# Performance work log

Hardware: AMD Instinct MI355X
Metric: run time of the kernel (lower is better)

The kernel has to match this reference:

```python
import jax, jax.numpy as jnp
import numpy as np

B_, C, N, M, DX = 4, 8, 1024, 1024, 1
POINTS_PER_UNIT = 64


def setup_inputs() -> dict:
    key = jax.random.key(0)
    k1, k2, k3 = jax.random.split(key, 3)
    xz = jax.random.uniform(k1, (M, DX), dtype=jnp.float32)          # grid locations
    z = jax.random.normal(k2, (B_, C, M, M), dtype=jnp.float32)      # grid encoding
    x = jax.random.normal(k3, (B_, N, DX), dtype=jnp.float32)        # target locations
    log_scale = jnp.log(jnp.float32(2.0 / POINTS_PER_UNIT))          # learned scalar
    return {"xz": xz, "z": z, "x": x, "log_scale": log_scale}


def reference(xz, z, x, log_scale):
    # pairwise squared distances: (b, n, m)
    dists2 = jnp.sum((x[:, :, None, :] - xz[None, None, :, :]) ** 2, axis=-1)
    # RBF weights
    weights = jnp.exp(-0.5 * dists2 / jnp.exp(2.0 * log_scale))      # (b, n, m)
    # weighted interpolation of grid encoding: (b, c, n, m)
    z1 = jnp.einsum("bnm,bcmk->bcnk", weights, z)
    # outer product z1 @ z1^T: (b, c, n, n)
    z2 = jnp.einsum("bcnk,bcok->bcno", z1, z1)
    return (xz, z2)
```

## Files before the change

kernel.cpp:

```cpp
#include <hip/hip_runtime.h>
#include <hip/hip_bf16.h>


typedef __attribute__((ext_vector_type(8))) unsigned short u16x8;
typedef __attribute__((ext_vector_type(8))) __bf16 bf16x8;
typedef __attribute__((ext_vector_type(4))) float f32x4;

typedef __attribute__((address_space(1))) void gvoid;
typedef __attribute__((address_space(3))) void svoid;
#define GLDS(g, s) __builtin_amdgcn_global_load_lds((gvoid*)(g), (svoid*)(s), 16, 0, 0)
#define BAR() asm volatile("s_barrier" ::: "memory")

__device__ __forceinline__ unsigned short f2bf(float f) {
  unsigned int u = __builtin_bit_cast(unsigned int, f);
  u += 0x7fffu + ((u >> 16) & 1u);
  return (unsigned short)(u >> 16);
}

__device__ __forceinline__ bf16x8 as_bf16x8(u16x8 v) {
  return __builtin_bit_cast(bf16x8, v);
}

__global__ void weights_kernel(const float* __restrict__ xz, const float* __restrict__ x,
                               const float* __restrict__ ls, unsigned short* __restrict__ W) {
  int bn = blockIdx.x;
  float xv = x[bn];
  float coef = -0.5f * __expf(-2.0f * ls[0]);
  unsigned short* Wrow = W + (size_t)bn * 1024;
  #pragma unroll
  for (int i = 0; i < 4; ++i) {
    int m = threadIdx.x + i * 256;
    float d = xv - xz[m];
    Wrow[m] = f2bf(__expf(coef * d * d));
  }
}

__global__ void transpose_kernel(const float* __restrict__ Z, unsigned short* __restrict__ Zt) {
  __shared__ float tile[64][65];
  int bc = blockIdx.z;
  const float* Zp = Z + ((size_t)bc << 20);
  unsigned short* Ztp = Zt + ((size_t)bc << 20);
  int m0 = blockIdx.x * 64, k0 = blockIdx.y * 64;
  int tx = threadIdx.x & 63, tg = threadIdx.x >> 6;
  #pragma unroll
  for (int i = 0; i < 16; ++i) {
    int ml = tg + i * 4;
    tile[ml][tx] = Zp[(size_t)(m0 + ml) * 1024 + k0 + tx];
  }
  __syncthreads();
  int tx2 = (threadIdx.x & 31) * 2, kg = threadIdx.x >> 5;
  #pragma unroll
  for (int i = 0; i < 8; ++i) {
    int kl = kg + i * 8;
    ushort2 v;
    v.x = f2bf(tile[tx2][kl]);
    v.y = f2bf(tile[tx2 + 1][kl]);
    *(ushort2*)&Ztp[(size_t)(k0 + kl) * 1024 + m0 + tx2] = v;
  }
}

template<bool A_PER_B>
__global__ __launch_bounds__(512, 2)
void gemm_nt8(const unsigned short* __restrict__ A, const unsigned short* __restrict__ B,
              unsigned short* __restrict__ Cbf) {
  extern __shared__ __align__(16) char smem[];

  const int bid = blockIdx.x;
  const int w = ((bid & 7) << 6) + (bid >> 3);
  const int bc = w >> 4;
  const int t  = w & 15;
  const int bi = t & 3, bj = t >> 2;

  const unsigned short* Ap = A + ((size_t)(A_PER_B ? (bc >> 3) : bc) << 20);
  const unsigned short* Bp = B + ((size_t)bc << 20);
  const int tid = threadIdx.x;
  const int wv = tid >> 6, lane = tid & 63;
  const int wr = wv >> 2, wc = wv & 3;
  const int la = lane & 15, ha = lane >> 4;

  f32x4 acc[8][4] = {};

  const int slog = (lane & 7) ^ (lane >> 3);
  const int rloc = 2 * (lane >> 3) + (slog & 1);
  const int cloc = (slog >> 1) * 8;
  const unsigned short* gA0 = Ap + (size_t)(bi*256 +       wv*16 + rloc) * 1024 + cloc;
  const unsigned short* gA1 = Ap + (size_t)(bi*256 + 128 + wv*16 + rloc) * 1024 + cloc;
  const unsigned short* gB0 = Bp + (size_t)(bj*256 +       wv*16 + rloc) * 1024 + cloc;
  const unsigned short* gB1 = Bp + (size_t)(bj*256 + 128 + wv*16 + rloc) * 1024 + cloc;
  const int ldsw = wv * 1024;

  auto stageA = [&](int d, int kh, int kt) {
    const int ko = kt * 64 + kh * 32;
    char* dst = smem + d * 32768 + kh * 16384 + ldsw;
    GLDS(gA0 + ko, dst); GLDS(gA1 + ko, dst + 8192);
  };
  auto stageB = [&](int d, int kh, int kt) {
    const int ko = kt * 64 + kh * 32;
    char* dst = smem + 65536 + d * 32768 + kh * 16384 + ldsw;
    GLDS(gB0 + ko, dst); GLDS(gB1 + ko, dst + 8192);
  };

  const int sphys = ((ha << 1) | (la & 1)) ^ (la >> 1);
  const int abase = wr * 8192 + (la >> 1) * 128 + sphys * 16;
  const int bbase = 65536 + wc * 4096 + (la >> 1) * 128 + sphys * 16;

  u16x8 aX[4], aY[4], b0[4], b1[4];
  auto lda4 = [&](u16x8* dst, int d, int kh, int ms) {
    const char* p = smem + d * 32768 + kh * 16384 + ms * 4096 + abase;
    dst[0] = *(const u16x8*)(p);
    dst[1] = *(const u16x8*)(p + 1024);
    dst[2] = *(const u16x8*)(p + 2048);
    dst[3] = *(const u16x8*)(p + 3072);
  };
  auto ldb4 = [&](u16x8* dst, int d, int kh) {
    const char* p = smem + d * 32768 + kh * 16384 + bbase;
    dst[0] = *(const u16x8*)(p);
    dst[1] = *(const u16x8*)(p + 1024);
    dst[2] = *(const u16x8*)(p + 2048);
    dst[3] = *(const u16x8*)(p + 3072);
  };
  auto mfma16 = [&](const u16x8* Af, const u16x8* Bf, int ms) {
    __builtin_amdgcn_s_setprio(1);
    #pragma unroll
    for (int i = 0; i < 4; ++i)
      #pragma unroll
      for (int n = 0; n < 4; ++n)
        acc[ms * 4 + i][n] = __builtin_amdgcn_mfma_f32_16x16x32_bf16(
            as_bf16x8(Af[i]), as_bf16x8(Bf[n]), acc[ms * 4 + i][n], 0, 0, 0);
    __builtin_amdgcn_s_setprio(0);
  };

  stageA(0, 0, 0); stageB(0, 0, 0);
  stageA(0, 1, 0); stageB(0, 1, 0);
  stageA(1, 0, 1); stageB(1, 0, 1);
  asm volatile("s_waitcnt vmcnt(8)" ::: "memory");
  BAR();
  ldb4(b0, 0, 0); lda4(aX, 0, 0, 0);

  for (int tt = 0; tt < 14; ++tt) {
    const int d = tt & 1;
    stageA(d ^ 1, 1, tt + 1);
    lda4(aY, d, 0, 1);
    mfma16(aX, b0, 0);
    stageB(d ^ 1, 1, tt + 1);
    asm volatile("s_waitcnt vmcnt(8)" ::: "memory");
    BAR();
    ldb4(b1, d, 1); lda4(aX, d, 1, 0);
    mfma16(aY, b0, 1);
    stageA(d, 0, tt + 2);
    lda4(aY, d, 1, 1);
    mfma16(aX, b1, 0);
    stageB(d, 0, tt + 2);
    asm volatile("s_waitcnt vmcnt(8)" ::: "memory");
    BAR();
    ldb4(b0, d ^ 1, 0); lda4(aX, d ^ 1, 0, 0);
    mfma16(aY, b1, 1);
  }
  stageA(1, 1, 15);
  lda4(aY, 0, 0, 1);
  mfma16(aX, b0, 0);
  stageB(1, 1, 15);
  asm volatile("s_waitcnt vmcnt(8)" ::: "memory");
  BAR();
  ldb4(b1, 0, 1); lda4(aX, 0, 1, 0);
  mfma16(aY, b0, 1);
  lda4(aY, 0, 1, 1);
  mfma16(aX, b1, 0);
  asm volatile("s_waitcnt vmcnt(4)" ::: "memory");
  BAR();
  ldb4(b0, 1, 0); lda4(aX, 1, 0, 0);
  mfma16(aY, b1, 1);
  lda4(aY, 1, 0, 1);
  mfma16(aX, b0, 0);
  asm volatile("s_waitcnt vmcnt(0)" ::: "memory");
  BAR();
  ldb4(b1, 1, 1); lda4(aX, 1, 1, 0);
  mfma16(aY, b0, 1);
  lda4(aY, 1, 1, 1);
  mfma16(aX, b1, 0);
  mfma16(aY, b1, 1);
  BAR();

  const size_t cb20 = (size_t)bc << 20;
  unsigned short* sE = (unsigned short*)(smem) + wv * 1152;
  const int r2 = lane >> 2, ch = lane & 3;
  #pragma unroll
  for (int mb = 0; mb < 8; ++mb) {
    #pragma unroll
    for (int nb = 0; nb < 4; ++nb)
      #pragma unroll
      for (int j = 0; j < 4; ++j)
        sE[(ha * 4 + j) * 72 + nb * 16 + la] = f2bf(acc[mb][nb][j]);
    u16x8 v0 = *(const u16x8*)&sE[r2 * 72 + ch * 16];
    u16x8 v1 = *(const u16x8*)&sE[r2 * 72 + ch * 16 + 8];
    unsigned short* gp = Cbf + cb20 +
        (size_t)(bi * 256 + wr * 128 + mb * 16 + r2) * 1024 + bj * 256 + wc * 64 + ch * 16;
    *(u16x8*)gp = v0;
    *(u16x8*)(gp + 8) = v1;
  }
}

__global__ __launch_bounds__(256, 3)
void gemm2_sym(const unsigned short* __restrict__ A, float* __restrict__ Cf) {
  __shared__ __align__(16) char smem[49152];

  const int chunk = 144;
  int w = ((int)blockIdx.x & 7) * chunk + ((int)blockIdx.x >> 3);
  int bc = w / 36;
  int t  = w % 36;
  int bi = 0;
  while (t >= 8 - bi) { t -= 8 - bi; ++bi; }
  int bj = bi + t;

  const unsigned short* Ap = A + ((size_t)bc << 20);
  const int tid = threadIdx.x;
  const int wave = tid >> 6, lane = tid & 63;
  const int wr = wave >> 1, wc = wave & 1;
  const int la = lane & 15, ha = lane >> 4;
  f32x4 acc[4][4] = {};

  const int slog = (lane & 7) ^ ((lane >> 3) & 7);
  const int rloc = 2 * (lane >> 3) + (slog & 1);
  const int cloc = (slog >> 1) * 8;
  const unsigned short* gA0 = Ap + (size_t)(bi * 128 + (wave * 2)     * 16 + rloc) * 1024 + cloc;
  const unsigned short* gA1 = Ap + (size_t)(bi * 128 + (wave * 2 + 1) * 16 + rloc) * 1024 + cloc;
  const unsigned short* gB0 = Ap + (size_t)(bj * 128 + (wave * 2)     * 16 + rloc) * 1024 + cloc;
  const unsigned short* gB1 = Ap + (size_t)(bj * 128 + (wave * 2 + 1) * 16 + rloc) * 1024 + cloc;

  auto stage = [&](int slot, int kt) {
    char* dA = smem + slot * 8192 + wave * 2048;
    char* dB = smem + 24576 + slot * 8192 + wave * 2048;
    GLDS(gA0 + kt, dA); GLDS(gA1 + kt, dA + 1024);
    GLDS(gB0 + kt, dB); GLDS(gB1 + kt, dB + 1024);
  };

  const int sphys = ((ha << 1) | (la & 1)) ^ (la >> 1);
  const int aoff = wr * 4096 + (la >> 1) * 128 + sphys * 16;
  const int boff = wc * 4096 + (la >> 1) * 128 + sphys * 16;

  auto compute = [&](int slot) {
    const char* rA = smem + slot * 8192;
    const char* rB = smem + 24576 + slot * 8192;
    u16x8 af[4], bfr[4];
    #pragma unroll
    for (int m = 0; m < 4; ++m) af[m]  = *(const u16x8*)(rA + aoff + m * 1024);
    #pragma unroll
    for (int n = 0; n < 4; ++n) bfr[n] = *(const u16x8*)(rB + boff + n * 1024);
    #pragma unroll
    for (int m = 0; m < 4; ++m)
      #pragma unroll
      for (int n = 0; n < 4; ++n)
        acc[m][n] = __builtin_amdgcn_mfma_f32_16x16x32_bf16(
            as_bf16x8(af[m]), as_bf16x8(bfr[n]), acc[m][n], 0, 0, 0);
  };

  stage(0, 0);
  stage(1, 32);
  asm volatile("s_waitcnt vmcnt(4)" ::: "memory");
  __builtin_amdgcn_s_barrier();
  int sl0 = 0, sl1 = 1, sl2 = 2;
  for (int t2 = 0; t2 < 32; ++t2) {
    if (t2 < 30) stage(sl2, (t2 + 2) * 32);
    compute(sl0);
    if (t2 < 30)       asm volatile("s_waitcnt vmcnt(4)" ::: "memory");
    else if (t2 == 30) asm volatile("s_waitcnt vmcnt(0)" ::: "memory");
    if (t2 < 31) __builtin_amdgcn_s_barrier();
    int tmp = sl0; sl0 = sl1; sl1 = sl2; sl2 = tmp;
  }
  __builtin_amdgcn_s_barrier();

  const size_t cb20 = (size_t)bc << 20;

  #pragma unroll
  for (int m = 0; m < 4; ++m) {
    int row0 = bi * 128 + wr * 64 + m * 16 + ha * 4;
    #pragma unroll
    for (int n = 0; n < 4; ++n) {
      int col = bj * 128 + wc * 64 + n * 16 + la;
      #pragma unroll
      for (int j = 0; j < 4; ++j)
        Cf[cb20 + (size_t)(row0 + j) * 1024 + col] = acc[m][n][j];
    }
  }
  if (bi != bj) {
    float (*sT)[129] = (float(*)[129])smem;
    #pragma unroll
    for (int b = 0; b < 4; ++b) {
      if (wr == (b >> 1)) {
        #pragma unroll
        for (int dm = 0; dm < 2; ++dm) {
          int m = (b & 1) * 2 + dm;
          #pragma unroll
          for (int n = 0; n < 4; ++n)
            #pragma unroll
            for (int j = 0; j < 4; ++j)
              sT[dm * 16 + ha * 4 + j][wc * 64 + n * 16 + la] = acc[m][n][j];
        }
      }
      __syncthreads();
      int c  = tid >> 1;
      int r0 = (tid & 1) * 16;
      float* gp = Cf + cb20 + (size_t)(bj * 128 + c) * 1024 + bi * 128 + b * 32 + r0;
      #pragma unroll
      for (int q = 0; q < 4; ++q) {
        f32x4 v;
        #pragma unroll
        for (int k = 0; k < 4; ++k) v[k] = sT[r0 + q * 4 + k][c];
        *(f32x4*)(gp + q * 4) = v;
      }
      __syncthreads();
    }
  }
}

extern "C" void kernel_launch(void* const* d_in, const int* in_sizes, int n_in,
                              void* d_out, int out_size, void* d_ws, size_t ws_size,
                              hipStream_t stream) {
  const float* xz = (const float*)d_in[0];
  const float* z  = (const float*)d_in[1];
  const float* x  = (const float*)d_in[2];
  const float* ls = (const float*)d_in[3];
  float* out = (float*)d_out;

  unsigned short* W  = (unsigned short*)d_ws;
  unsigned short* Zt = W + ((size_t)4 << 20);
  unsigned short* z1 = Zt + ((size_t)32 << 20);

  hipFuncSetAttribute((const void*)gemm_nt8<true>,
                      hipFuncAttributeMaxDynamicSharedMemorySize, 131072);

  hipMemcpyAsync(out, xz, 1024 * sizeof(float), hipMemcpyDeviceToDevice, stream);
  weights_kernel<<<4096, 256, 0, stream>>>(xz, x, ls, W);
  transpose_kernel<<<dim3(16, 16, 32), 256, 0, stream>>>(z, Zt);
  gemm_nt8<true><<<512, 512, 131072, stream>>>(W, Zt, z1);
  gemm2_sym<<<32 * 36, 256, 0, stream>>>(z1, out + 1024);
}
```

Before: 172.8 us.

## Double-buffer LDS fragment reads in registers and raise MFMA priority in GEMM loop

The main GEMM loop now issues LDS reads for the next k-step into a second register set while the MFMAs for the current step run, using ping-pong register fragments and a three-slot LDS ring that is prefetched three tiles deep. MFMA bursts are wrapped in s_setprio to favour the matrix pipe across waves. The goal is to hide LDS read latency behind MFMA work and keep one barrier per k-step. It costs extra VGPRs for the second fragment set, which could lower occupancy, and the hand-scheduled slot rotation and wait counts are fragile.

```diff
diff --git a/kernel.cpp b/kernel.cpp
--- a/kernel.cpp
+++ b/kernel.cpp
@@ -236,38 +236,66 @@
 
   const int sphys = ((ha << 1) | (la & 1)) ^ (la >> 1);
   const int aoff = wr * 4096 + (la >> 1) * 128 + sphys * 16;
-  const int boff = wc * 4096 + (la >> 1) * 128 + sphys * 16;
-
-  auto compute = [&](int slot) {
-    const char* rA = smem + slot * 8192;
-    const char* rB = smem + 24576 + slot * 8192;
-    u16x8 af[4], bfr[4];
-    #pragma unroll
-    for (int m = 0; m < 4; ++m) af[m]  = *(const u16x8*)(rA + aoff + m * 1024);
-    #pragma unroll
-    for (int n = 0; n < 4; ++n) bfr[n] = *(const u16x8*)(rB + boff + n * 1024);
+  const int boff = 24576 + wc * 4096 + (la >> 1) * 128 + sphys * 16;
+
+  u16x8 aX[4], bX[4], aY[4], bY[4];
+  auto rd = [&](u16x8* da, u16x8* db, int slot) {
+    const char* pa = smem + slot * 8192 + aoff;
+    const char* pb = smem + slot * 8192 + boff;
+    da[0] = *(const u16x8*)(pa);
+    da[1] = *(const u16x8*)(pa + 1024);
+    da[2] = *(const u16x8*)(pa + 2048);
+    da[3] = *(const u16x8*)(pa + 3072);
+    db[0] = *(const u16x8*)(pb);
+    db[1] = *(const u16x8*)(pb + 1024);
+    db[2] = *(const u16x8*)(pb + 2048);
+    db[3] = *(const u16x8*)(pb + 3072);
+  };
+  auto mfma16 = [&](const u16x8* Af, const u16x8* Bf) {
+    __builtin_amdgcn_s_setprio(1);
     #pragma unroll
     for (int m = 0; m < 4; ++m)
       #pragma unroll
       for (int n = 0; n < 4; ++n)
         acc[m][n] = __builtin_amdgcn_mfma_f32_16x16x32_bf16(
-            as_bf16x8(af[m]), as_bf16x8(bfr[n]), acc[m][n], 0, 0, 0);
-  };
-
-  stage(0, 0);
-  stage(1, 32);
+            as_bf16x8(Af[m]), as_bf16x8(Bf[n]), acc[m][n], 0, 0, 0);
+    __builtin_amdgcn_s_setprio(0);
+  };
+
+  stage(0, 0); stage(1, 32); stage(2, 64);
   asm volatile("s_waitcnt vmcnt(4)" ::: "memory");
-  __builtin_amdgcn_s_barrier();
-  int sl0 = 0, sl1 = 1, sl2 = 2;
-  for (int t2 = 0; t2 < 32; ++t2) {
-    if (t2 < 30) stage(sl2, (t2 + 2) * 32);
-    compute(sl0);
-    if (t2 < 30)       asm volatile("s_waitcnt vmcnt(4)" ::: "memory");
-    else if (t2 == 30) asm volatile("s_waitcnt vmcnt(0)" ::: "memory");
-    if (t2 < 31) __builtin_amdgcn_s_barrier();
-    int tmp = sl0; sl0 = sl1; sl1 = sl2; sl2 = tmp;
-  }
-  __builtin_amdgcn_s_barrier();
+  BAR();
+  rd(aX, bX, 0);
+  asm volatile("s_waitcnt lgkmcnt(0)" ::: "memory");
+  BAR();
+
+  int p0 = 0, p1 = 1, p2 = 2;
+  for (int t2 = 0; t2 < 28; t2 += 2) {
+    stage(p0, (t2 + 3) * 32);
+    rd(aY, bY, p1);
+    mfma16(aX, bX);
+    asm volatile("s_waitcnt vmcnt(4)" ::: "memory");
+    BAR();
+    stage(p1, (t2 + 4) * 32);
+    rd(aX, bX, p2);
+    mfma16(aY, bY);
+    asm volatile("s_waitcnt vmcnt(4)" ::: "memory");
+    BAR();
+    int tmp = p2; p2 = p1; p1 = p0; p0 = tmp;
+  }
+  stage(p0, 31 * 32);
+  rd(aY, bY, p1);
+  mfma16(aX, bX);
+  asm volatile("s_waitcnt vmcnt(4)" ::: "memory");
+  BAR();
+  rd(aX, bX, p2);
+  mfma16(aY, bY);
+  asm volatile("s_waitcnt vmcnt(0)" ::: "memory");
+  BAR();
+  rd(aY, bY, p0);
+  mfma16(aX, bX);
+  mfma16(aY, bY);
+  BAR();
 
   const size_t cb20 = (size_t)bc << 20;
 
```

After: 171.7 us. No clear change (-0.6%).
